# Optimization experiments

Measured on AMD Instinct MI355X. Metric: run time of the kernel, lower is better.

## Reference

```python
import jax, jax.numpy as jnp
import numpy as np

N_NODES = 50000
N_EDGES = 1_600_000
F = 64      # num_edge_features
NH = 3      # n_h hidden blocks
BN_EPS = 1e-5


def setup_inputs() -> dict:
    key = jax.random.key(0)
    ks = jax.random.split(key, 8)
    edge_attr = jax.random.normal(ks[0], (N_EDGES, F), jnp.float32)
    nbr_shift = 0.1 * jax.random.normal(ks[1], (N_EDGES, 3), jnp.float32)
    pos = 10.0 * jax.random.normal(ks[2], (N_NODES, 3), jnp.float32)
    edge_index = jax.random.randint(ks[3], (2, N_EDGES), 0, N_NODES, dtype=jnp.int64)
    Ws = jax.random.normal(ks[4], (NH, F, F), jnp.float32) / np.sqrt(F).astype(np.float32)
    bs = jnp.zeros((NH, F), jnp.float32)
    gammas = jnp.ones((NH, F), jnp.float32)
    betas = jnp.zeros((NH, F), jnp.float32)
    w_out = jax.random.normal(ks[5], (F,), jnp.float32) / np.sqrt(F).astype(np.float32)
    b_out = jnp.zeros((1,), jnp.float32)
    return {"edge_attr": edge_attr, "nbr_shift": nbr_shift, "pos": pos,
            "Ws": Ws, "bs": bs, "gammas": gammas, "betas": betas,
            "w_out": w_out, "b_out": b_out, "edge_index": edge_index}


def _batchnorm(x, gamma, beta):
    # training-mode BatchNorm1d: batch mean / biased variance over edges
    mu = jnp.mean(x, axis=0)
    var = jnp.mean(jnp.square(x - mu), axis=0)
    return gamma * (x - mu) * jax.lax.rsqrt(var + BN_EPS) + beta


def reference(edge_attr, nbr_shift, pos, Ws, bs, gammas, betas, w_out, b_out, edge_index):
    j = edge_index[0]  # source atoms
    i = edge_index[1]  # target atoms
    # gather positions by edge, normalized edge direction  [E,3]
    edge_dir = pos[i] + nbr_shift - pos[j]
    edge_len = jnp.sqrt(jnp.sum(jnp.square(edge_dir), axis=-1, keepdims=True))
    edge_dir = edge_dir / edge_len
    h = edge_attr
    for l in range(NH):
        h = _batchnorm(h @ Ws[l] + bs[l], gammas[l], betas[l])
        h = jax.nn.softplus(h)
    s = (h @ w_out)[:, None] + b_out  # [E,1] scalar per edge
    force_e = s * edge_dir            # [E,3]
    # scatter-add edge forces onto target atoms
    force = jax.ops.segment_sum(force_e, i, num_segments=N_NODES)  # [N,3]
    return force
```

## Files before the change

kernel.cpp:

```cpp
#include <hip/hip_runtime.h>
#include <hip/hip_bf16.h>
#include <math.h>

#define F 64
#define TPB 256
#define MTILE 256
#define BN_EPS 1e-5f
#define LGRID 512
#define NREP 8

typedef __attribute__((ext_vector_type(8))) short short8;
typedef __attribute__((ext_vector_type(4))) float f32x4;

__device__ __forceinline__ float sp(float x) {
    return fmaxf(x, 0.f) + __logf(1.f + __expf(-fabsf(x)));
}
__device__ __forceinline__ ushort f2bf(float f) {
    __hip_bfloat16 h = __float2bfloat16(f);
    return *reinterpret_cast<ushort*>(&h);
}
__device__ __forceinline__ float bf2f(ushort u) {
    unsigned v = ((unsigned)u) << 16;
    return __builtin_bit_cast(float, v);
}

template <int HAS_ACT>
__global__ __launch_bounds__(TPB, 2)
void layer_mfma(const void* __restrict__ Xv, uint2* __restrict__ Yg,
                const float* __restrict__ W,
                const float* __restrict__ prev_stats,
                const float* __restrict__ gamma_prev,
                const float* __restrict__ beta_prev,
                float* __restrict__ stats_out, int E)
{
    __shared__ short8 Wt[512];
    __shared__ float aca[F], acb[F];
    __shared__ float sh_s[F], sh_q[F];

    const int t  = threadIdx.x;
    const int w  = t >> 6;
    const int l  = t & 63;
    const int ln = l & 15;
    const int q  = l >> 4;

    #pragma unroll
    for (int uu = 0; uu < 2; ++uu) {
        int u = t + uu * 256;
        int kq = u >> 6, n = u & 63;
        short8 pk;
        #pragma unroll
        for (int j = 0; j < 8; ++j)
            pk[j] = (short)f2bf(W[(kq * 8 + j) * F + n]);
        Wt[u] = pk;
    }
    if (t < F) {
        sh_s[t] = 0.f; sh_q[t] = 0.f;
        if (HAS_ACT) {
            float inv_e = 1.f / (float)E;
            float mu = prev_stats[t] * inv_e;
            float var = prev_stats[F + t] * inv_e - mu * mu;
            float a = gamma_prev[t] * rsqrtf(var + BN_EPS);
            aca[t] = a;
            acb[t] = beta_prev[t] - mu * a;
        }
    }
    __syncthreads();

    short8 afr[4][2];
    #pragma unroll
    for (int ni = 0; ni < 4; ++ni)
        #pragma unroll
        for (int ks = 0; ks < 2; ++ks)
            afr[ni][ks] = Wt[(4 * ks + q) * 64 + ni * 16 + ln];

    float ps[16], pq[16];
    #pragma unroll
    for (int p = 0; p < 16; ++p) { ps[p] = 0.f; pq[p] = 0.f; }

    const int ntiles = E >> 8;

    auto store_acc = [&](f32x4 (&acc)[4][4], int tt) {
        const long e0 = (long)tt * MTILE + w * 64;
        #pragma unroll
        for (int ni = 0; ni < 4; ++ni)
            #pragma unroll
            for (int mi = 0; mi < 4; ++mi) {
                const long e = e0 + mi * 16 + ln;
                f32x4 v = acc[ni][mi];
                uint2 u;
                u.x = (uint)f2bf(v[0]) | ((uint)f2bf(v[1]) << 16);
                u.y = (uint)f2bf(v[2]) | ((uint)f2bf(v[3]) << 16);
                Yg[(size_t)(ni * 4 + q) * E + e] = u;
                #pragma unroll
                for (int r = 0; r < 4; ++r) {
                    float x = v[r];
                    ps[ni * 4 + r] += x;
                    pq[ni * 4 + r] = fmaf(x, x, pq[ni * 4 + r]);
                }
            }
    };

    if constexpr (HAS_ACT) {
        const uint2* X = (const uint2*)Xv;
        uint2 xbA[4][2][2], xbB[4][2][2];

        auto load = [&](uint2 (&xb)[4][2][2], int tt) {
            const long eb = (long)tt * MTILE + w * 64;
            #pragma unroll
            for (int mi = 0; mi < 4; ++mi) {
                const long e = eb + mi * 16 + ln;
                #pragma unroll
                for (int ks = 0; ks < 2; ++ks) {
                    xb[mi][ks][0] = X[(size_t)(8 * ks + 2 * q) * E + e];
                    xb[mi][ks][1] = X[(size_t)(8 * ks + 2 * q + 1) * E + e];
                }
            }
        };

        auto process = [&](uint2 (&xb)[4][2][2], int tt) {
            f32x4 acc[4][4];
            #pragma unroll
            for (int ni = 0; ni < 4; ++ni)
                #pragma unroll
                for (int mi = 0; mi < 4; ++mi)
                    acc[ni][mi] = (f32x4){0.f, 0.f, 0.f, 0.f};

            #pragma unroll
            for (int mi = 0; mi < 4; ++mi) {
                short8 bfr[2];
                #pragma unroll
                for (int ks = 0; ks < 2; ++ks) {
                    uint vs[4] = {xb[mi][ks][0].x, xb[mi][ks][0].y,
                                  xb[mi][ks][1].x, xb[mi][ks][1].y};
                    short8 b;
                    #pragma unroll
                    for (int d = 0; d < 4; ++d) {
                        float x0 = bf2f((ushort)(vs[d] & 0xffffu));
                        float x1 = bf2f((ushort)(vs[d] >> 16));
                        int k0 = 32 * ks + 8 * q + 2 * d;
                        b[2*d]   = (short)f2bf(sp(aca[k0]     * x0 + acb[k0]));
                        b[2*d+1] = (short)f2bf(sp(aca[k0 + 1] * x1 + acb[k0 + 1]));
                    }
                    bfr[ks] = b;
                }
                #pragma unroll
                for (int ks = 0; ks < 2; ++ks)
                    #pragma unroll
                    for (int ni = 0; ni < 4; ++ni)
                        acc[ni][mi] = __builtin_amdgcn_mfma_f32_16x16x32_bf16(
                                          afr[ni][ks], bfr[ks], acc[ni][mi], 0, 0, 0);
            }
            store_acc(acc, tt);
        };

        int tile = blockIdx.x;
        load(xbA, tile);
        while (true) {
            const int tB = tile + LGRID;
            const bool haveB = tB < ntiles;
            if (haveB) load(xbB, tB);
            process(xbA, tile);
            if (!haveB) break;
            tile = tB + LGRID;
            if (tile < ntiles) load(xbA, tile);
            process(xbB, tB);
            if (tile >= ntiles) break;
        }
    } else {
        const float4* X4 = (const float4*)Xv;
        float4 xb[4][2][2];

        auto load = [&](int tt) {
            const long eb = (long)tt * MTILE + w * 64;
            #pragma unroll
            for (int mi = 0; mi < 4; ++mi) {
                const long e = eb + mi * 16 + ln;
                #pragma unroll
                for (int ks = 0; ks < 2; ++ks) {
                    xb[mi][ks][0] = X4[(size_t)e * 16 + 8 * ks + 2 * q];
                    xb[mi][ks][1] = X4[(size_t)e * 16 + 8 * ks + 2 * q + 1];
                }
            }
        };

        load(blockIdx.x);
        #pragma unroll 1
        for (int tile = blockIdx.x; tile < ntiles; tile += LGRID) {
            short8 bfr[4][2];
            #pragma unroll
            for (int mi = 0; mi < 4; ++mi)
                #pragma unroll
                for (int ks = 0; ks < 2; ++ks) {
                    float4 f0 = xb[mi][ks][0], f1 = xb[mi][ks][1];
                    short8 b;
                    b[0] = (short)f2bf(f0.x); b[1] = (short)f2bf(f0.y);
                    b[2] = (short)f2bf(f0.z); b[3] = (short)f2bf(f0.w);
                    b[4] = (short)f2bf(f1.x); b[5] = (short)f2bf(f1.y);
                    b[6] = (short)f2bf(f1.z); b[7] = (short)f2bf(f1.w);
                    bfr[mi][ks] = b;
                }
            if (tile + LGRID < ntiles) load(tile + LGRID);

            f32x4 acc[4][4];
            #pragma unroll
            for (int ni = 0; ni < 4; ++ni)
                #pragma unroll
                for (int mi = 0; mi < 4; ++mi)
                    acc[ni][mi] = (f32x4){0.f, 0.f, 0.f, 0.f};
            #pragma unroll
            for (int mi = 0; mi < 4; ++mi)
                #pragma unroll
                for (int ks = 0; ks < 2; ++ks)
                    #pragma unroll
                    for (int ni = 0; ni < 4; ++ni)
                        acc[ni][mi] = __builtin_amdgcn_mfma_f32_16x16x32_bf16(
                                          afr[ni][ks], bfr[mi][ks], acc[ni][mi], 0, 0, 0);
            store_acc(acc, tile);
        }
    }

    #pragma unroll
    for (int p = 0; p < 16; ++p) {
        #pragma unroll
        for (int m = 1; m < 16; m <<= 1) {
            ps[p] += __shfl_xor(ps[p], m);
            pq[p] += __shfl_xor(pq[p], m);
        }
    }
    if (ln == 0) {
        #pragma unroll
        for (int p = 0; p < 16; ++p) {
            int n = (p >> 2) * 16 + q * 4 + (p & 3);
            atomicAdd(&sh_s[n], ps[p]);
            atomicAdd(&sh_q[n], pq[p]);
        }
    }
    __syncthreads();
    if (t < F) {
        unsafeAtomicAdd(&stats_out[t], sh_s[t]);
        unsafeAtomicAdd(&stats_out[F + t], sh_q[t]);
    }
}

__global__ __launch_bounds__(TPB)
void force_kernel(const uint2* __restrict__ Yg, const float* __restrict__ stats,
                  const float* __restrict__ gamma, const float* __restrict__ beta,
                  const float* __restrict__ w_out, const float* __restrict__ b_out,
                  const float* __restrict__ nbr_shift, const float* __restrict__ pos,
                  const int* __restrict__ edge_index, float* __restrict__ rep,
                  int E, int nodes3)
{
    __shared__ float ac[2 * F];
    __shared__ float wsh[F];
    const int t = threadIdx.x;
    if (t < F) {
        float inv_e = 1.f / (float)E;
        float mu = stats[t] * inv_e;
        float var = stats[F + t] * inv_e - mu * mu;
        float a = gamma[t] * rsqrtf(var + BN_EPS);
        ac[t] = a;
        ac[F + t] = beta[t] - mu * a;
        wsh[t] = w_out[t];
    }
    __syncthreads();

    const long e = (long)blockIdx.x * TPB + t;
    if (e >= E) return;

    float s = b_out[0];
    #pragma unroll
    for (int nq = 0; nq < 16; ++nq) {
        uint2 u = Yg[(size_t)nq * E + e];
        int k = 4 * nq;
        float x0 = bf2f((ushort)(u.x & 0xffffu));
        float x1 = bf2f((ushort)(u.x >> 16));
        float x2 = bf2f((ushort)(u.y & 0xffffu));
        float x3 = bf2f((ushort)(u.y >> 16));
        s = fmaf(sp(ac[k]     * x0 + ac[F + k]),     wsh[k],     s);
        s = fmaf(sp(ac[k + 1] * x1 + ac[F + k + 1]), wsh[k + 1], s);
        s = fmaf(sp(ac[k + 2] * x2 + ac[F + k + 2]), wsh[k + 2], s);
        s = fmaf(sp(ac[k + 3] * x3 + ac[F + k + 3]), wsh[k + 3], s);
    }

    const int jn  = edge_index[e];
    const int in_ = edge_index[E + e];
    float dx = pos[3 * in_ + 0] + nbr_shift[3 * e + 0] - pos[3 * jn + 0];
    float dy = pos[3 * in_ + 1] + nbr_shift[3 * e + 1] - pos[3 * jn + 1];
    float dz = pos[3 * in_ + 2] + nbr_shift[3 * e + 2] - pos[3 * jn + 2];
    float inv = rsqrtf(dx * dx + dy * dy + dz * dz);
    float fs = s * inv;

    float* myrep = rep + (size_t)(blockIdx.x & (NREP - 1)) * nodes3;
    unsafeAtomicAdd(&myrep[3 * in_ + 0], fs * dx);
    unsafeAtomicAdd(&myrep[3 * in_ + 1], fs * dy);
    unsafeAtomicAdd(&myrep[3 * in_ + 2], fs * dz);
}

__global__ __launch_bounds__(TPB)
void reduce_out(const float* __restrict__ rep, float* __restrict__ out, int nodes3)
{
    const int i = blockIdx.x * TPB + threadIdx.x;
    if (i >= nodes3) return;
    float s = 0.f;
    #pragma unroll
    for (int r = 0; r < NREP; ++r)
        s += rep[(size_t)r * nodes3 + i];
    out[i] = s;
}

extern "C" void kernel_launch(void* const* d_in, const int* in_sizes, int n_in,
                              void* d_out, int out_size, void* d_ws, size_t ws_size,
                              hipStream_t stream)
{
    const int E = in_sizes[0] / F;
    const float* edge_attr = (const float*)d_in[0];
    const float* nbr_shift = (const float*)d_in[1];
    const float* pos       = (const float*)d_in[2];
    const float* Ws        = (const float*)d_in[3];
    const float* gammas    = (const float*)d_in[5];
    const float* betas     = (const float*)d_in[6];
    const float* w_out     = (const float*)d_in[7];
    const float* b_out     = (const float*)d_in[8];
    const int*   edge_index= (const int*)d_in[9];

    uint2* Y1 = (uint2*)d_ws;
    uint2* Y2 = (uint2*)((char*)d_ws + (size_t)E * F * 2);
    float* stats = (float*)((char*)d_ws + (size_t)E * F * 4);
    float* rep   = (float*)((char*)d_ws + (size_t)E * F * 4 + 4096);

    hipMemsetAsync(stats, 0, 6 * F * sizeof(float), stream);
    hipMemsetAsync(rep, 0, (size_t)NREP * out_size * sizeof(float), stream);

    layer_mfma<0><<<LGRID, TPB, 0, stream>>>(edge_attr, Y1, Ws,
                                             nullptr, nullptr, nullptr, stats, E);
    layer_mfma<1><<<LGRID, TPB, 0, stream>>>(Y1, Y2, Ws + F * F,
                                             stats, gammas, betas, stats + 2 * F, E);
    layer_mfma<1><<<LGRID, TPB, 0, stream>>>(Y2, Y1, Ws + 2 * F * F,
                                             stats + 2 * F, gammas + F, betas + F,
                                             stats + 4 * F, E);
    force_kernel<<<E / TPB, TPB, 0, stream>>>(Y1, stats + 4 * F, gammas + 2 * F,
                                              betas + 2 * F, w_out, b_out,
                                              nbr_shift, pos, edge_index, rep,
                                              E, out_size);
    reduce_out<<<(out_size + TPB - 1) / TPB, TPB, 0, stream>>>(rep, (float*)d_out,
                                                               out_size);
}
```

Baseline: 1.037 ms.

## Replace global atomic scatter with node-range bucketing and LDS accumulation

Instead of scattering per-edge forces straight into replicated global arrays with atomics, the force kernel now writes each edge's force and target index as a record into one of 16 node-range buckets. A second kernel accumulates each bucket in shared memory across 16 sub-blocks and writes partial slabs, which a final reduce sums along with an overflow spill array. This swaps scattered global atomics for one extra pass of coalesced record writes and reads plus LDS atomics, and relies on a fixed bucket capacity that falls back to global atomics on overflow.

```diff
diff --git a/kernel.cpp b/kernel.cpp
--- a/kernel.cpp
+++ b/kernel.cpp
@@ -7,7 +7,12 @@
 #define MTILE 256
 #define BN_EPS 1e-5f
 #define LGRID 512
-#define NREP 8
+
+#define NB 16
+#define RMAX 3136
+#define CAP 114688
+#define BPB 16
+#define SLABSTRIDE (3 * RMAX)
 
 typedef __attribute__((ext_vector_type(8))) short short8;
 typedef __attribute__((ext_vector_type(4))) float f32x4;
@@ -243,15 +248,17 @@
 }
 
 __global__ __launch_bounds__(TPB)
-void force_kernel(const uint2* __restrict__ Yg, const float* __restrict__ stats,
+void force_bucket(const uint2* __restrict__ Yg, const float* __restrict__ stats,
                   const float* __restrict__ gamma, const float* __restrict__ beta,
                   const float* __restrict__ w_out, const float* __restrict__ b_out,
                   const float* __restrict__ nbr_shift, const float* __restrict__ pos,
-                  const int* __restrict__ edge_index, float* __restrict__ rep,
-                  int E, int nodes3)
+                  const int* __restrict__ edge_index,
+                  float4* __restrict__ recs, int* __restrict__ gcnt,
+                  float* __restrict__ spill, int E, int R)
 {
     __shared__ float ac[2 * F];
     __shared__ float wsh[F];
+    __shared__ int lcnt[NB], lbase[NB];
     const int t = threadIdx.x;
     if (t < F) {
         float inv_e = 1.f / (float)E;
@@ -262,49 +269,102 @@
         ac[F + t] = beta[t] - mu * a;
         wsh[t] = w_out[t];
     }
+    if (t < NB) lcnt[t] = 0;
     __syncthreads();
 
     const long e = (long)blockIdx.x * TPB + t;
-    if (e >= E) return;
-
-    float s = b_out[0];
-    #pragma unroll
-    for (int nq = 0; nq < 16; ++nq) {
-        uint2 u = Yg[(size_t)nq * E + e];
-        int k = 4 * nq;
-        float x0 = bf2f((ushort)(u.x & 0xffffu));
-        float x1 = bf2f((ushort)(u.x >> 16));
-        float x2 = bf2f((ushort)(u.y & 0xffffu));
-        float x3 = bf2f((ushort)(u.y >> 16));
-        s = fmaf(sp(ac[k]     * x0 + ac[F + k]),     wsh[k],     s);
-        s = fmaf(sp(ac[k + 1] * x1 + ac[F + k + 1]), wsh[k + 1], s);
-        s = fmaf(sp(ac[k + 2] * x2 + ac[F + k + 2]), wsh[k + 2], s);
-        s = fmaf(sp(ac[k + 3] * x3 + ac[F + k + 3]), wsh[k + 3], s);
-    }
-
-    const int jn  = edge_index[e];
-    const int in_ = edge_index[E + e];
-    float dx = pos[3 * in_ + 0] + nbr_shift[3 * e + 0] - pos[3 * jn + 0];
-    float dy = pos[3 * in_ + 1] + nbr_shift[3 * e + 1] - pos[3 * jn + 1];
-    float dz = pos[3 * in_ + 2] + nbr_shift[3 * e + 2] - pos[3 * jn + 2];
-    float inv = rsqrtf(dx * dx + dy * dy + dz * dz);
-    float fs = s * inv;
-
-    float* myrep = rep + (size_t)(blockIdx.x & (NREP - 1)) * nodes3;
-    unsafeAtomicAdd(&myrep[3 * in_ + 0], fs * dx);
-    unsafeAtomicAdd(&myrep[3 * in_ + 1], fs * dy);
-    unsafeAtomicAdd(&myrep[3 * in_ + 2], fs * dz);
+    const bool valid = e < E;
+    float4 rec;
+    int b = 0, lrank = 0, in_ = 0;
+
+    if (valid) {
+        float s = b_out[0];
+        #pragma unroll
+        for (int nq = 0; nq < 16; ++nq) {
+            uint2 u = Yg[(size_t)nq * E + e];
+            int k = 4 * nq;
+            float x0 = bf2f((ushort)(u.x & 0xffffu));
+            float x1 = bf2f((ushort)(u.x >> 16));
+            float x2 = bf2f((ushort)(u.y & 0xffffu));
+            float x3 = bf2f((ushort)(u.y >> 16));
+            s = fmaf(sp(ac[k]     * x0 + ac[F + k]),     wsh[k],     s);
+            s = fmaf(sp(ac[k + 1] * x1 + ac[F + k + 1]), wsh[k + 1], s);
+            s = fmaf(sp(ac[k + 2] * x2 + ac[F + k + 2]), wsh[k + 2], s);
+            s = fmaf(sp(ac[k + 3] * x3 + ac[F + k + 3]), wsh[k + 3], s);
+        }
+
+        const int jn = edge_index[e];
+        in_ = edge_index[E + e];
+        float dx = pos[3 * in_ + 0] + nbr_shift[3 * e + 0] - pos[3 * jn + 0];
+        float dy = pos[3 * in_ + 1] + nbr_shift[3 * e + 1] - pos[3 * jn + 1];
+        float dz = pos[3 * in_ + 2] + nbr_shift[3 * e + 2] - pos[3 * jn + 2];
+        float inv = rsqrtf(dx * dx + dy * dy + dz * dz);
+        float fs = s * inv;
+        rec.x = fs * dx; rec.y = fs * dy; rec.z = fs * dz;
+        rec.w = __int_as_float(in_);
+
+        b = (int)((unsigned)in_ / (unsigned)R);
+        lrank = atomicAdd(&lcnt[b], 1);
+    }
+    __syncthreads();
+    if (t < NB) lbase[t] = atomicAdd(&gcnt[t], lcnt[t]);
+    __syncthreads();
+    if (valid) {
+        int idx = lbase[b] + lrank;
+        if (idx < CAP) {
+            recs[(size_t)b * CAP + idx] = rec;
+        } else {
+            unsafeAtomicAdd(&spill[3 * in_ + 0], rec.x);
+            unsafeAtomicAdd(&spill[3 * in_ + 1], rec.y);
+            unsafeAtomicAdd(&spill[3 * in_ + 2], rec.z);
+        }
+    }
 }
 
 __global__ __launch_bounds__(TPB)
-void reduce_out(const float* __restrict__ rep, float* __restrict__ out, int nodes3)
+void bucket_accum(const float4* __restrict__ recs, const int* __restrict__ gcnt,
+                  float* __restrict__ slabs, int R)
+{
+    __shared__ float acc[SLABSTRIDE];
+    const int bucket = blockIdx.x / BPB;
+    const int sub    = blockIdx.x - bucket * BPB;
+    const int t = threadIdx.x;
+    const int len = 3 * R;
+
+    for (int i = t; i < len; i += TPB) acc[i] = 0.f;
+    __syncthreads();
+
+    int cnt = gcnt[bucket];
+    if (cnt > CAP) cnt = CAP;
+    const int nbase = bucket * R;
+    const float4* rb = recs + (size_t)bucket * CAP;
+
+    for (int i = sub * TPB + t; i < cnt; i += BPB * TPB) {
+        float4 r = rb[i];
+        int loc = 3 * (__float_as_int(r.w) - nbase);
+        atomicAdd(&acc[loc + 0], r.x);
+        atomicAdd(&acc[loc + 1], r.y);
+        atomicAdd(&acc[loc + 2], r.z);
+    }
+    __syncthreads();
+
+    float* out = slabs + (size_t)blockIdx.x * SLABSTRIDE;
+    for (int i = t; i < len; i += TPB) out[i] = acc[i];
+}
+
+__global__ __launch_bounds__(TPB)
+void reduce_out(const float* __restrict__ slabs, const float* __restrict__ spill,
+                float* __restrict__ out, int nodes3, int R)
 {
     const int i = blockIdx.x * TPB + threadIdx.x;
     if (i >= nodes3) return;
-    float s = 0.f;
+    const int node = i / 3, c = i - 3 * node;
+    const int bucket = node / R, loc = node - bucket * R;
+    const size_t off = (size_t)(bucket * BPB) * SLABSTRIDE + 3 * loc + c;
+    float s = spill[i];
     #pragma unroll
-    for (int r = 0; r < NREP; ++r)
-        s += rep[(size_t)r * nodes3 + i];
+    for (int r = 0; r < BPB; ++r)
+        s += slabs[off + (size_t)r * SLABSTRIDE];
     out[i] = s;
 }
 
@@ -323,13 +383,23 @@
     const float* b_out     = (const float*)d_in[8];
     const int*   edge_index= (const int*)d_in[9];
 
-    uint2* Y1 = (uint2*)d_ws;
-    uint2* Y2 = (uint2*)((char*)d_ws + (size_t)E * F * 2);
-    float* stats = (float*)((char*)d_ws + (size_t)E * F * 4);
-    float* rep   = (float*)((char*)d_ws + (size_t)E * F * 4 + 4096);
+    const int nodes3 = out_size;
+    const int nodes  = nodes3 / 3;
+    const int R = (nodes + NB - 1) / NB;
+
+    char* p = (char*)d_ws;
+    const size_t SZY = (size_t)E * F * 2;
+    uint2* Y1 = (uint2*)p;                 p += SZY;
+    uint2* Y2 = (uint2*)p;                 p += SZY;
+    float* stats = (float*)p;              p += 4096;
+    float4* recs = (float4*)p;             p += (size_t)NB * CAP * 16;
+    int*   gcnt  = (int*)p;                p += 256;
+    float* slabs = (float*)p;              p += (size_t)NB * BPB * SLABSTRIDE * 4;
+    float* spill = (float*)p;              p += (size_t)nodes3 * 4;
 
     hipMemsetAsync(stats, 0, 6 * F * sizeof(float), stream);
-    hipMemsetAsync(rep, 0, (size_t)NREP * out_size * sizeof(float), stream);
+    hipMemsetAsync(gcnt, 0, 256, stream);
+    hipMemsetAsync(spill, 0, (size_t)nodes3 * sizeof(float), stream);
 
     layer_mfma<0><<<LGRID, TPB, 0, stream>>>(edge_attr, Y1, Ws,
                                              nullptr, nullptr, nullptr, stats, E);
@@ -338,10 +408,10 @@
     layer_mfma<1><<<LGRID, TPB, 0, stream>>>(Y2, Y1, Ws + 2 * F * F,
                                              stats + 2 * F, gammas + F, betas + F,
                                              stats + 4 * F, E);
-    force_kernel<<<E / TPB, TPB, 0, stream>>>(Y1, stats + 4 * F, gammas + 2 * F,
-                                              betas + 2 * F, w_out, b_out,
-                                              nbr_shift, pos, edge_index, rep,
-                                              E, out_size);
-    reduce_out<<<(out_size + TPB - 1) / TPB, TPB, 0, stream>>>(rep, (float*)d_out,
-                                                               out_size);
-}
+    force_bucket<<<(E + TPB - 1) / TPB, TPB, 0, stream>>>(
+        Y1, stats + 4 * F, gammas + 2 * F, betas + 2 * F, w_out, b_out,
+        nbr_shift, pos, edge_index, recs, gcnt, spill, E, R);
+    bucket_accum<<<NB * BPB, TPB, 0, stream>>>(recs, gcnt, slabs, R);
+    reduce_out<<<(nodes3 + TPB - 1) / TPB, TPB, 0, stream>>>(
+        slabs, spill, (float*)d_out, nodes3, R);
+}
```

After: 924.6 us. 1.12x faster.
